# Performance work log

Measured on AMD Instinct MI355X. Metric: run time of the kernel, lower is better.

## Reference

```python
import jax, jax.numpy as jnp
from jax import lax
import numpy as np

EPS = 2.220446049250313e-16  # sys.float_info.epsilon


def setup_inputs() -> dict:
    key = jax.random.key(0)
    k1, k2, k3, k4 = jax.random.split(key, 4)
    C, H, W, R = 256, 256, 256, 16
    x = jax.random.normal(k1, (1, C, H, W), dtype=jnp.float32)
    w1 = jax.random.normal(k2, (R, C), dtype=jnp.float32) * 0.05   # Linear(C -> C//r), no bias
    w2 = jax.random.normal(k3, (C, R), dtype=jnp.float32) * 0.05   # Linear(C//r -> C), no bias
    conv_w = jax.random.normal(k4, (1, 2, 7, 7), dtype=jnp.float32) * 0.05  # Conv2d(2,1,7)
    return {"x": x, "w1": w1, "w2": w2, "conv_w": conv_w, "kv": 1}


def reference(x, w1, w2, conv_w, kv):
    b, c, h, w = x.shape  # b == 1 (module assumes batch 1 via squeeze(0))

    def fc(v):  # shared MLP of the channel attention
        return jnp.maximum(v @ w1.T, 0.0) @ w2.T

    y_avg = fc(x.mean(axis=(2, 3)))          # [1, C]
    y_max = fc(x.max(axis=(2, 3)))           # [1, C]
    y = jax.nn.sigmoid(y_avg + y_max)        # [1, C]

    yc = y[0]
    yc = (yc - yc.min()) / (yc.max() - yc.min() + 1e-20)  # min-max normalized gates in [0,1]

    # Batched SVD over channels replaces the per-channel Python loop.
    mats = x[0]                                            # [C, H, W]
    u, s, vh = jnp.linalg.svd(mats, full_matrices=False)   # u:[C,H,K] s:[C,K] vh:[C,K,W]
    K = s.shape[-1]
    # k = int(len(s) * kv * yc[c]); singular values are sorted descending, so
    # top-k selection == keep the first k -> mask the tail.
    k = jnp.floor(K * kv * yc).astype(jnp.int32)           # [C]
    keep = jnp.arange(K)[None, :] < k[:, None]             # [C, K]
    s_m = jnp.where(keep, s, 0.0)
    recon = jnp.einsum('chk,ck,ckw->chw', u, s_m, vh)      # low-rank reconstruction
    x2 = recon[None]                                       # [1, C, H, W]

    avg_out = x2.mean(axis=1, keepdims=True)
    max_out = x2.max(axis=1, keepdims=True)
    cat = jnp.concatenate([avg_out, max_out], axis=1)      # [1, 2, H, W]
    out = lax.conv_general_dilated(cat, conv_w, (1, 1), [(3, 3), (3, 3)],
                                   dimension_numbers=('NCHW', 'OIHW', 'NCHW'))
    out = jnp.where(out < EPS, EPS, out)
    return jax.nn.sigmoid(out)
```

## Files before the change

### kernel.cpp

```cpp
#include <hip/hip_runtime.h>


#define NCH 256
#define N 256
#define NN 65536
#define NS_MAX 22

#define OFF_K 0
#define OFF_MODE 256
#define OFF_MC 512
#define OFF_COEF 768
#define OFF_SUM 12032
#define OFF_MAXHW 77568
#define OFF_MEAND 143104
#define OFF_MAXD 143616
#define OFF_T 144128
#define OFF_ALPHA 144640
#define OFF_AQ 145152
#define OFF_BQ 276224
#define OFF_ITSW 407296
#define SMALL_FLOATS 407552

#define NSH_LDS 135168
#define F16_PANEL 33792

#define P_TOTAL 33280

static const float EPSF = 2.220446049250313e-16f;

typedef unsigned short u16;
typedef _Float16 h8 __attribute__((ext_vector_type(8)));
typedef float f32x4 __attribute__((ext_vector_type(4)));

__device__ __forceinline__ float rdlane(float v, int l) {
  return __uint_as_float(__builtin_amdgcn_readlane(__float_as_uint(v), l));
}

__device__ __forceinline__ int offP(int rr) {
  int q = rr >> 2, s = rr & 3;
  return 4 * (q + 1) * (2 * q + s);
}

__device__ __forceinline__ u16 f2h(float v) {
  _Float16 h = (_Float16)v;
  u16 u;
  __builtin_memcpy(&u, &h, 2);
  return u;
}
__device__ __forceinline__ float h2f(u16 u) {
  _Float16 h;
  __builtin_memcpy(&h, &u, 2);
  return (float)h;
}

__device__ __forceinline__ double block_sum1024d(double v, double* red, int tid) {
  for (int off = 32; off; off >>= 1) v += __shfl_down(v, off, 64);
  __syncthreads();
  if ((tid & 63) == 0) red[tid >> 6] = v;
  __syncthreads();
  double s = 0.0;
#pragma unroll
  for (int i = 0; i < 16; ++i) s += red[i];
  return s;
}

__global__ __launch_bounds__(256) void k_chan_stats(const float* __restrict__ x,
                                                    float* __restrict__ small) {
  int c = blockIdx.x, tid = threadIdx.x;
  const float4* xc = (const float4*)(x + (size_t)c * NN);
  double s = 0.0;
  float m = -1e30f;
  for (int i = tid; i < NN / 4; i += 256) {
    float4 v = xc[i];
    s += (double)v.x + (double)v.y + (double)v.z + (double)v.w;
    m = fmaxf(m, fmaxf(fmaxf(v.x, v.y), fmaxf(v.z, v.w)));
  }
  __shared__ double rs[4];
  __shared__ float rm[4];
  for (int off = 32; off; off >>= 1) {
    s += __shfl_down(s, off, 64);
    m = fmaxf(m, __shfl_down(m, off, 64));
  }
  if ((tid & 63) == 0) { rs[tid >> 6] = s; rm[tid >> 6] = m; }
  __syncthreads();
  if (tid == 0) {
    ((double*)(small + OFF_MEAND))[c] = (rs[0] + rs[1] + rs[2] + rs[3]) / (double)NN;
    ((double*)(small + OFF_MAXD))[c] =
        (double)fmaxf(fmaxf(rm[0], rm[1]), fmaxf(rm[2], rm[3]));
  }
}

__global__ __launch_bounds__(256) void k_attention(const float* __restrict__ w1,
                                                   const float* __restrict__ w2,
                                                   const int* __restrict__ kvp,
                                                   float* __restrict__ small) {
  int tid = threadIdx.x;
  __shared__ double ha[16], hm[16], redd[8], ymn[256], ymx[256];
  double va = ((const double*)(small + OFF_MEAND))[tid];
  double vm = ((const double*)(small + OFF_MAXD))[tid];
  for (int r = 0; r < 16; ++r) {
    double wv = (double)w1[r * 256 + tid];
    double pa = wv * va, pm = wv * vm;
    for (int off = 32; off; off >>= 1) {
      pa += __shfl_down(pa, off, 64);
      pm += __shfl_down(pm, off, 64);
    }
    if ((tid & 63) == 0) { redd[tid >> 6] = pa; redd[4 + (tid >> 6)] = pm; }
    __syncthreads();
    if (tid == 0) {
      ha[r] = fmax(redd[0] + redd[1] + redd[2] + redd[3], 0.0);
      hm[r] = fmax(redd[4] + redd[5] + redd[6] + redd[7], 0.0);
    }
    __syncthreads();
  }
  double ya = 0.0, ym = 0.0;
  for (int r = 0; r < 16; ++r) {
    double wv = (double)w2[tid * 16 + r];
    ya += ha[r] * wv;
    ym += hm[r] * wv;
  }
  double y = 1.0 / (1.0 + exp(-(ya + ym)));
  ymn[tid] = y; ymx[tid] = y;
  __syncthreads();
  for (int off = 128; off; off >>= 1) {
    if (tid < off) {
      ymn[tid] = fmin(ymn[tid], ymn[tid + off]);
      ymx[tid] = fmax(ymx[tid], ymx[tid + off]);
    }
    __syncthreads();
  }
  double yc = (y - ymn[0]) / (ymx[0] - ymn[0] + 1e-20);
  int kv = kvp[0];
  int k = (int)floor(256.0 * (double)kv * yc);
  int mode = (k <= 0) ? 0 : ((k >= 256) ? 1 : 2);
  int* ip = (int*)small;
  ip[OFF_K + tid] = k;
  ip[OFF_MODE + tid] = mode;
}

#define GEMM128_VARS                                                           \
  int tid = threadIdx.x;                                                       \
  int tx4 = (tid & 15) * 4, ty4 = (tid >> 4) * 4;                              \
  int lm = tid >> 1, lq = (tid & 1) * 2;                                       \
  int lk = tid >> 4, lc = (tid & 15) * 2;                                      \
  (void)lk; (void)lc;

#define STORE_T128(Ls, v0, v1)                                                 \
  Ls[lq * 4 + 0][lm] = v0.x; Ls[lq * 4 + 1][lm] = v0.y;                        \
  Ls[lq * 4 + 2][lm] = v0.z; Ls[lq * 4 + 3][lm] = v0.w;                        \
  Ls[lq * 4 + 4][lm] = v1.x; Ls[lq * 4 + 5][lm] = v1.y;                        \
  Ls[lq * 4 + 6][lm] = v1.z; Ls[lq * 4 + 7][lm] = v1.w;

#define GEMM128_INNER(AsM, BsM)                                                \
  _Pragma("unroll") for (int kk = 0; kk < 16; ++kk) {                          \
    float4 a0 = *(const float4*)&AsM[kk][ty4];                                 \
    float4 a1 = *(const float4*)&AsM[kk][64 + ty4];                            \
    float4 b0 = *(const float4*)&BsM[kk][tx4];                                 \
    float4 b1 = *(const float4*)&BsM[kk][64 + tx4];                            \
    float av[8] = {a0.x, a0.y, a0.z, a0.w, a1.x, a1.y, a1.z, a1.w};            \
    float bv[8] = {b0.x, b0.y, b0.z, b0.w, b1.x, b1.y, b1.z, b1.w};            \
    _Pragma("unroll") for (int rr = 0; rr < 8; ++rr)                           \
      _Pragma("unroll") for (int cc2 = 0; cc2 < 8; ++cc2)                      \
        acc[rr][cc2] += av[rr] * bv[cc2];                                      \
  }

#define WRITE_TILE_NORM(Cc)                                                    \
  _Pragma("unroll") for (int rh = 0; rh < 2; ++rh)                             \
  _Pragma("unroll") for (int rr = 0; rr < 4; ++rr) {                           \
    int rI = rh * 4 + rr;                                                      \
    float* rowp = (Cc) + (size_t)(i0 + rh * 64 + ty4 + rr) * N + j0;           \
    *(float4*)(rowp + tx4) =                                                   \
        make_float4(acc[rI][0], acc[rI][1], acc[rI][2], acc[rI][3]);           \
    *(float4*)(rowp + 64 + tx4) =                                              \
        make_float4(acc[rI][4], acc[rI][5], acc[rI][6], acc[rI][7]);           \
  }

#define WRITE_TILE_MIRROR(Cc)                                                  \
  _Pragma("unroll") for (int ch = 0; ch < 2; ++ch)                             \
  _Pragma("unroll") for (int cc2 = 0; cc2 < 4; ++cc2) {                        \
    int cI = ch * 4 + cc2;                                                     \
    float* rowp = (Cc) + (size_t)(j0 + ch * 64 + tx4 + cc2) * N + i0;          \
    *(float4*)(rowp + ty4) =                                                   \
        make_float4(acc[0][cI], acc[1][cI], acc[2][cI], acc[3][cI]);           \
    *(float4*)(rowp + 64 + ty4) =                                              \
        make_float4(acc[4][cI], acc[5][cI], acc[6][cI], acc[7][cI]);           \
  }

#define SYM_MAP                                                                \
  int bx = blockIdx.x;                                                         \
  int i0 = (bx >= 1) ? 128 : 0, j0 = (bx == 2) ? 128 : 0;

__global__ __launch_bounds__(256) void k_gram(const float* __restrict__ x,
                                              float* __restrict__ bufA, int base) {
  __shared__ float As[16][132], Bs[16][132];
  GEMM128_VARS; SYM_MAP;
  const float* A = x + (size_t)(base + blockIdx.z) * NN;
  float acc[8][8] = {};
  const float* Ap = A + (size_t)(i0 + lm) * N + lq * 4;
  const float* Bp = A + (size_t)(j0 + lm) * N + lq * 4;
  float4 va0 = *(const float4*)Ap, va1 = *(const float4*)(Ap + 4);
  float4 vb0 = *(const float4*)Bp, vb1 = *(const float4*)(Bp + 4);
  for (int kt = 0; kt < 16; ++kt) {
    __syncthreads();
    STORE_T128(As, va0, va1); STORE_T128(Bs, vb0, vb1);
    __syncthreads();
    if (kt < 15) {
      va0 = *(const float4*)(Ap + (kt + 1) * 16);
      va1 = *(const float4*)(Ap + (kt + 1) * 16 + 4);
      vb0 = *(const float4*)(Bp + (kt + 1) * 16);
      vb1 = *(const float4*)(Bp + (kt + 1) * 16 + 4);
    }
    GEMM128_INNER(As, Bs);
  }
  float* Cc = bufA + (size_t)blockIdx.z * NN;
  WRITE_TILE_NORM(Cc);
  if (bx == 1) { WRITE_TILE_MIRROR(Cc); }
}

__global__ __launch_bounds__(1024) void k_tridiag(const float* __restrict__ Gall,
                                                  float* __restrict__ small, int base) {
  extern __shared__ double dls[];
  double* redd = dls;
  double* wd = dls + 16;
  double* pip = dls + 272;
  float* P = (float*)(dls + 1296);
  float* uf = P + P_TOTAL;
  int tid = threadIdx.x, lane = tid & 63;
  int r = tid & 255, g = tid >> 8;
  int R0 = ((tid >> 6) & 3) << 6;
  int c = base + blockIdx.x;
  const int* ip = (const int*)small;
  if (ip[OFF_MODE + c] != 2) return;
  const float* G = Gall + (size_t)blockIdx.x * NN;
  double* aq = (double*)(small + OFF_AQ) + (size_t)c * 256;
  double* bq = (double*)(small + OFF_BQ) + (size_t)c * 256;
  const int offR = offP(r);

  for (int i = g; i < N; i += 4)
    if (r <= i) P[offP(i) + r] = G[i * N + r];
  __syncthreads();

  for (int j = 0; j + 2 < N; ++j) {
    if (g == 0 && r >= j + 1) uf[r] = P[offR + j];
    __syncthreads();
    float ur0 = uf[r];
    double part = (g == 0 && r >= j + 2) ? (double)ur0 * (double)ur0 : 0.0;
    double x0 = (double)uf[j + 1];
    double sigma = block_sum1024d(part, redd, tid);
    if (sigma <= 1e-40) {
      if (tid == 0) bq[j] = x0;
      __syncthreads();
      continue;
    }
    double nu = sqrt(x0 * x0 + sigma);
    double bsub = (x0 >= 0.0) ? -nu : nu;
    double beta = 1.0 / (nu * (nu + fabs(x0)));
    if (tid == j + 1) uf[tid] = (float)(x0 - bsub);
    __syncthreads();
    int cbase = (j + 1) & ~63;
    int c0 = cbase + 64 * g;
    float ureg = 0.f;
    if (c0 < N) ureg = uf[c0 + lane];
    double myp = 0.0;
    if (c0 < N) {
      int lbeg = (c0 > j + 1) ? c0 : (j + 1);
      int lend = c0 + 64;
      if (lbeg < lend) {
        double pi0 = 0.0, pi1 = 0.0, pi2 = 0.0, pi3 = 0.0;
        if (c0 + 64 <= R0) {
          int lmv = lbeg;
          for (; lmv < lend && (lmv & 3); ++lmv) {
            float uv = rdlane(ureg, lmv - c0);
            pi0 += (double)P[offR + lmv] * (double)uv;
          }
          for (; lmv + 3 < lend; lmv += 4) {
            float4 v4 = *(const float4*)&P[offR + lmv];
            float uv0 = rdlane(ureg, lmv - c0), uv1 = rdlane(ureg, lmv + 1 - c0);
            float uv2 = rdlane(ureg, lmv + 2 - c0), uv3 = rdlane(ureg, lmv + 3 - c0);
            pi0 += (double)v4.x * (double)uv0;
            pi1 += (double)v4.y * (double)uv1;
            pi2 += (double)v4.z * (double)uv2;
            pi3 += (double)v4.w * (double)uv3;
          }
        } else if (c0 >= R0 + 64) {
          int lmv = lbeg;
          int oL = offP(lbeg);
          for (; lmv + 3 < lend; lmv += 4) {
            int o0 = oL;
            int o1 = o0 + ((lmv + 4) & ~3);
            int o2 = o1 + ((lmv + 5) & ~3);
            int o3 = o2 + ((lmv + 6) & ~3);
            oL = o3 + ((lmv + 7) & ~3);
            float uv0 = rdlane(ureg, lmv - c0), uv1 = rdlane(ureg, lmv + 1 - c0);
            float uv2 = rdlane(ureg, lmv + 2 - c0), uv3 = rdlane(ureg, lmv + 3 - c0);
            pi0 += (double)P[o0 + r] * (double)uv0;
            pi1 += (double)P[o1 + r] * (double)uv1;
            pi2 += (double)P[o2 + r] * (double)uv2;
            pi3 += (double)P[o3 + r] * (double)uv3;
          }
          for (; lmv < lend; ++lmv) {
            float uv = rdlane(ureg, lmv - c0);
            pi0 += (double)P[oL + r] * (double)uv;
            oL += (lmv + 4) & ~3;
          }
        } else {
          for (int lmv = lbeg; lmv < lend; ++lmv) {
            float uv = rdlane(ureg, lmv - c0);
            float v = P[(lmv <= r) ? (offR + lmv) : (offP(lmv) + r)];
            pi0 += (double)v * (double)uv;
          }
        }
        myp = (pi0 + pi1) + (pi2 + pi3);
      }
    }
    pip[tid] = (r >= j + 1) ? myp : 0.0;
    __syncthreads();
    double ur = (r >= j + 1) ? (double)uf[r] : 0.0;
    double pi = 0.0;
    if (g == 0 && r >= j + 1)
      pi = (pip[r] + pip[256 + r] + pip[512 + r] + pip[768 + r]) * beta;
    double kpart = (g == 0) ? ur * pi : 0.0;
    double K = block_sum1024d(kpart, redd, tid) * beta * 0.5;
    if (g == 0) wd[r] = pi - K * ur;
    __syncthreads();
    if (c0 < N && r >= j + 1) {
      double wr = wd[r];
      int lbeg = (c0 > j + 1) ? c0 : (j + 1);
      int lend = c0 + 64;
      int lcap = (r | 63) + 1;
      if (lend > lcap) lend = lcap;
      if (c0 + 64 <= R0) {
        int lmv = lbeg;
        for (; lmv < lend && (lmv & 3); ++lmv) {
          double uv = (double)rdlane(ureg, lmv - c0), wv = wd[lmv];
          P[offR + lmv] = (float)((double)P[offR + lmv] - ur * wv - wr * uv);
        }
        for (; lmv + 3 < lend; lmv += 4) {
          float4 p4 = *(float4*)&P[offR + lmv];
          double uv0 = (double)rdlane(ureg, lmv - c0), wv0 = wd[lmv];
          double uv1 = (double)rdlane(ureg, lmv + 1 - c0), wv1 = wd[lmv + 1];
          double uv2 = (double)rdlane(ureg, lmv + 2 - c0), wv2 = wd[lmv + 2];
          double uv3 = (double)rdlane(ureg, lmv + 3 - c0), wv3 = wd[lmv + 3];
          p4.x = (float)((double)p4.x - ur * wv0 - wr * uv0);
          p4.y = (float)((double)p4.y - ur * wv1 - wr * uv1);
          p4.z = (float)((double)p4.z - ur * wv2 - wr * uv2);
          p4.w = (float)((double)p4.w - ur * wv3 - wr * uv3);
          *(float4*)&P[offR + lmv] = p4;
        }
      } else if (c0 == R0) {
        for (int lmv = lbeg; lmv < lend; ++lmv) {
          double uv = (double)rdlane(ureg, lmv - c0), wv = wd[lmv];
          if (lmv <= r)
            P[offR + lmv] = (float)((double)P[offR + lmv] - ur * wv - wr * uv);
        }
      }
    }
    if (tid == 0) bq[j] = bsub;
    __syncthreads();
  }
  if (g == 0) aq[r] = (double)P[offR + r];
  if (tid == 0) bq[N - 2] = (double)P[offP(N - 1) + N - 2];
}

__device__ __forceinline__ int sturm_count_lds(const double* a, const double* b,
                                               double t) {
  double d = a[0] - t;
  int cnt = (d < 0.0);
  for (int i = 1; i < N; ++i) {
    double den = d;
    if (fabs(den) < 1e-20) den = (den < 0.0) ? -1e-20 : 1e-20;
    double bb = b[i - 1];
    d = (a[i] - t) - bb * bb / den;
    cnt += (d < 0.0);
  }
  return cnt;
}

__global__ __launch_bounds__(64) void k_bisect(float* __restrict__ small,
                                               int base, int cc) {
  int ci = blockIdx.x;
  if (ci >= cc) return;
  int c = base + ci, lane = threadIdx.x;
  int* ip = (int*)small;
  if (ip[OFF_MODE + c] != 2) {
    if (lane == 0) { ip[OFF_MC + c] = 0; ip[OFF_ITSW + c] = 0; }
    return;
  }
  int k = ip[OFF_K + c];
  const double* a = (const double*)(small + OFF_AQ) + (size_t)c * 256;
  const double* b = (const double*)(small + OFF_BQ) + (size_t)c * 256;
  __shared__ double sa[256], sb[256];
  for (int i = lane; i < N; i += 64) {
    sa[i] = a[i];
    if (i < N - 1) sb[i] = b[i];
  }
  __syncthreads();
  double lo = 1e300, hi = -1e300;
  for (int i = lane; i < N; i += 64) {
    double rr = (i > 0 ? fabs(sb[i - 1]) : 0.0) + (i < N - 1 ? fabs(sb[i]) : 0.0);
    lo = fmin(lo, sa[i] - rr);
    hi = fmax(hi, sa[i] + rr);
  }
  for (int off = 32; off; off >>= 1) {
    lo = fmin(lo, __shfl_xor(lo, off, 64));
    hi = fmax(hi, __shfl_xor(hi, off, 64));
  }
  double lamk = 0.0, lamk1 = 0.0;
  for (int which = 0; which < 2; ++which) {
    int j = (which == 0) ? (N - k + 1) : (N - k);
    double l0 = lo, h0 = hi;
    for (int pass = 0; pass < 10; ++pass) {
      double step = (h0 - l0) * (1.0 / 65.0);
      double t = l0 + step * (double)(lane + 1);
      int cnt = sturm_count_lds(sa, sb, t);
      unsigned long long mask = __ballot(cnt >= j);
      if (mask == 0ull) {
        l0 = l0 + step * 64.0;
      } else {
        int bpos = __ffsll((long long)mask) - 1;
        double nl = (bpos == 0) ? l0 : (l0 + step * (double)bpos);
        h0 = l0 + step * (double)(bpos + 1);
        l0 = nl;
      }
    }
    double v = 0.5 * (l0 + h0);
    if (which == 0) lamk = v; else lamk1 = v;
  }
  if (lane == 0) {
    double t = 0.5 * (lamk + lamk1);
    double gap = fmax(lamk - lamk1, 0.0);
    double alpha = 1.002 * fmax(hi - t, t - lo) + 1e-30;
    double g0 = fmax(gap / (2.0 * alpha), 2e-6);
    float* cf = small + OFF_COEF + (size_t)c * (2 * NS_MAX);
    double l = fmin(g0, 0.99);
    int m = 0, isw = NS_MAX;
    while (m < NS_MAX - 2 && l < 0.9999) {
      if (isw == NS_MAX && l >= 0.04) isw = m;
      double aa = sqrt(27.0 / (4.0 * (1.0 + l + l * l)));
      double bb = (4.0 / 27.0) * aa * aa * aa;
      cf[2 * m] = (float)aa;
      cf[2 * m + 1] = (float)bb;
      double pl = aa * l - bb * l * l * l;
      double p1 = aa - bb;
      l = fmin(pl, p1);
      m++;
    }
    for (int e = 0; e < 2; ++e) {
      if (isw == NS_MAX && l >= 0.04) isw = m;
      cf[2 * m] = 1.5f; cf[2 * m + 1] = 0.5f; m++;
    }
    if (isw > m) isw = m;
    ip[OFF_MC + c] = m;
    ip[OFF_ITSW + c] = isw;
    ((double*)(small + OFF_T))[c] = t;
    ((double*)(small + OFF_ALPHA))[c] = alpha;
  }
}

__global__ void k_x0(const float* __restrict__ small, float* __restrict__ bufA,
                     int base) {
  int ci = blockIdx.y, c = base + ci;
  const int* ip = (const int*)small;
  if (ip[OFF_MODE + c] != 2) return;
  double t = ((const double*)(small + OFF_T))[c];
  double inva = 1.0 / ((const double*)(small + OFF_ALPHA))[c];
  float* X = bufA + (size_t)ci * NN;
  int r = blockIdx.x, tid = threadIdx.x;
  double gg = (double)X[r * N + tid];
  if (tid == r) gg -= t;
  X[r * N + tid] = (float)(gg * inva);
}

__global__ __launch_bounds__(256) void k_ns1(const float* __restrict__ src,
                                             float* __restrict__ Sb,
                                             const float* __restrict__ small,
                                             int base, int it) {
  const int* ip = (const int*)small;
  int c = base + blockIdx.z;
  if (ip[OFF_MODE + c] != 2 || it >= ip[OFF_ITSW + c]) return;
  __shared__ float As[16][132], Bs[16][132];
  GEMM128_VARS; SYM_MAP;
  const float* X = src + (size_t)blockIdx.z * NN;
  float acc[8][8] = {};
  const float* Ap = X + (size_t)(i0 + lm) * N + lq * 4;
  const float* Bp = X + (size_t)(j0 + lm) * N + lq * 4;
  float4 va0 = *(const float4*)Ap, va1 = *(const float4*)(Ap + 4);
  float4 vb0 = *(const float4*)Bp, vb1 = *(const float4*)(Bp + 4);
  for (int kt = 0; kt < 16; ++kt) {
    __syncthreads();
    STORE_T128(As, va0, va1); STORE_T128(Bs, vb0, vb1);
    __syncthreads();
    if (kt < 15) {
      va0 = *(const float4*)(Ap + (kt + 1) * 16);
      va1 = *(const float4*)(Ap + (kt + 1) * 16 + 4);
      vb0 = *(const float4*)(Bp + (kt + 1) * 16);
      vb1 = *(const float4*)(Bp + (kt + 1) * 16 + 4);
    }
    GEMM128_INNER(As, Bs);
  }
  float* Cc = Sb + (size_t)blockIdx.z * NN;
  WRITE_TILE_NORM(Cc);
  if (bx == 1) { WRITE_TILE_MIRROR(Cc); }
}

__global__ __launch_bounds__(256) void k_ns2(const float* __restrict__ src,
                                             const float* __restrict__ Sb,
                                             float* __restrict__ dst,
                                             const float* __restrict__ small,
                                             int base, int it) {
  const int* ip = (const int*)small;
  int c = base + blockIdx.z;
  if (ip[OFF_MODE + c] != 2 || it >= ip[OFF_ITSW + c]) return;
  float ca = small[OFF_COEF + (size_t)c * (2 * NS_MAX) + 2 * it];
  float cb = small[OFF_COEF + (size_t)c * (2 * NS_MAX) + 2 * it + 1];
  __shared__ float As[16][132], Bs[16][132];
  GEMM128_VARS; SYM_MAP;
  const float* X = src + (size_t)blockIdx.z * NN;
  const float* S = Sb + (size_t)blockIdx.z * NN;
  float acc[8][8] = {};
  const float* Ap = X + (size_t)(i0 + lm) * N + lq * 4;
  const float* Bp = S + (size_t)(j0 + lm) * N + lq * 4;
  float4 va0 = *(const float4*)Ap, va1 = *(const float4*)(Ap + 4);
  float4 vb0 = *(const float4*)Bp, vb1 = *(const float4*)(Bp + 4);
  for (int kt = 0; kt < 16; ++kt) {
    __syncthreads();
    STORE_T128(As, va0, va1); STORE_T128(Bs, vb0, vb1);
    __syncthreads();
    if (kt < 15) {
      va0 = *(const float4*)(Ap + (kt + 1) * 16);
      va1 = *(const float4*)(Ap + (kt + 1) * 16 + 4);
      vb0 = *(const float4*)(Bp + (kt + 1) * 16);
      vb1 = *(const float4*)(Bp + (kt + 1) * 16 + 4);
    }
    GEMM128_INNER(As, Bs);
  }
#pragma unroll
  for (int rh = 0; rh < 2; ++rh)
#pragma unroll
    for (int rr = 0; rr < 4; ++rr) {
      int rI = rh * 4 + rr;
      const float* rowp = X + (size_t)(i0 + rh * 64 + ty4 + rr) * N + j0;
      float4 x0 = *(const float4*)(rowp + tx4);
      float4 x1 = *(const float4*)(rowp + 64 + tx4);
      acc[rI][0] = ca * x0.x - cb * acc[rI][0];
      acc[rI][1] = ca * x0.y - cb * acc[rI][1];
      acc[rI][2] = ca * x0.z - cb * acc[rI][2];
      acc[rI][3] = ca * x0.w - cb * acc[rI][3];
      acc[rI][4] = ca * x1.x - cb * acc[rI][4];
      acc[rI][5] = ca * x1.y - cb * acc[rI][5];
      acc[rI][6] = ca * x1.z - cb * acc[rI][6];
      acc[rI][7] = ca * x1.w - cb * acc[rI][7];
    }
  float* Y = dst + (size_t)blockIdx.z * NN;
  WRITE_TILE_NORM(Y);
  if (bx == 1) { WRITE_TILE_MIRROR(Y); }
}

__device__ __forceinline__ void stage_h(u16* pan, const u16* g16, int tid) {
#pragma unroll
  for (int i = 0; i < 16; ++i) {
    int g = tid * 16 + i * 4096;
    int lo = g + ((g >> 9) << 4);
    *(uint4*)((char*)pan + lo) = *(const uint4*)((const char*)g16 + g);
  }
}
__device__ __forceinline__ void stage_f(u16* pan, const float* gF, int tid) {
#pragma unroll
  for (int i = 0; i < 16; ++i) {
    int e = tid * 8 + i * 2048;
    float4 v0 = *(const float4*)(gF + e);
    float4 v1 = *(const float4*)(gF + e + 4);
    h8 hv;
    hv[0] = (_Float16)v0.x; hv[1] = (_Float16)v0.y;
    hv[2] = (_Float16)v0.z; hv[3] = (_Float16)v0.w;
    hv[4] = (_Float16)v1.x; hv[5] = (_Float16)v1.y;
    hv[6] = (_Float16)v1.z; hv[7] = (_Float16)v1.w;
    int b = e * 2;
    int lo = b + ((b >> 9) << 4);
    *(h8*)((char*)pan + lo) = hv;
  }
}

__global__ __launch_bounds__(256) void k_nsh(const float* __restrict__ srcF,
                                             float* __restrict__ Sf,
                                             float* __restrict__ dstF,
                                             const float* __restrict__ small,
                                             int base, int it, int phase) {
  const int* ip = (const int*)small;
  int ci = blockIdx.z, c = base + ci;
  if (ip[OFF_MODE + c] != 2) return;
  int isw = ip[OFF_ITSW + c], mc = ip[OFF_MC + c];
  if (it < isw || it >= mc) return;
  SYM_MAP;
  extern __shared__ char ldsraw[];
  u16* Apan = (u16*)ldsraw;
  u16* Bpan = Apan + F16_PANEL;
  int tid = threadIdx.x;
  bool cvtA = (it == isw);
  bool sameP = (phase == 0) && (bx != 1);
  const float* XF = srcF + (size_t)ci * NN;
  const u16* XH = (const u16*)XF;
  if (cvtA) stage_f(Apan, XF + (size_t)i0 * N, tid);
  else      stage_h(Apan, XH + (size_t)i0 * N, tid);
  if (!sameP) {
    if (phase == 0) {
      if (cvtA) stage_f(Bpan, XF + (size_t)j0 * N, tid);
      else      stage_h(Bpan, XH + (size_t)j0 * N, tid);
    } else {
      const u16* SH = (const u16*)(Sf + (size_t)ci * NN);
      stage_h(Bpan, SH + (size_t)j0 * N, tid);
    }
  }
  const u16* Bb = sameP ? Apan : Bpan;
  __syncthreads();

  int l = tid & 63, wid = tid >> 6;
  int wr = (wid >> 1) * 64, wc = (wid & 1) * 64;
  int rA = wr + (l & 15), rB = wc + (l & 15);
  int kB = (l >> 4) << 3;
  f32x4 zero = {0.f, 0.f, 0.f, 0.f};
  f32x4 acc[4][4];
#pragma unroll
  for (int mi = 0; mi < 4; ++mi)
#pragma unroll
    for (int ni = 0; ni < 4; ++ni) acc[mi][ni] = zero;

#pragma unroll
  for (int kc = 0; kc < 8; ++kc) {
    int kof = kc * 32 + kB;
    h8 af[4], bf[4];
#pragma unroll
    for (int mi = 0; mi < 4; ++mi)
      af[mi] = *(const h8*)((const char*)Apan +
                            ((size_t)(rA + mi * 16) * 264 + kof) * 2);
#pragma unroll
    for (int ni = 0; ni < 4; ++ni)
      bf[ni] = *(const h8*)((const char*)Bb +
                            ((size_t)(rB + ni * 16) * 264 + kof) * 2);
#pragma unroll
    for (int mi = 0; mi < 4; ++mi)
#pragma unroll
      for (int ni = 0; ni < 4; ++ni)
        acc[mi][ni] = __builtin_amdgcn_mfma_f32_16x16x32_f16(
            af[mi], bf[ni], acc[mi][ni], 0, 0, 0);
  }

  float cav = 0.f, cbv = 0.f;
  bool last = false;
  if (phase) {
    cav = small[OFF_COEF + (size_t)c * (2 * NS_MAX) + 2 * it];
    cbv = small[OFF_COEF + (size_t)c * (2 * NS_MAX) + 2 * it + 1];
    last = (it == mc - 1);
  }
  float* oF = dstF + (size_t)ci * NN;
  u16* oH = phase ? (u16*)oF : (u16*)(Sf + (size_t)ci * NN);
  int lr4 = (l >> 4) << 2, lcn = l & 15;
#pragma unroll
  for (int mi = 0; mi < 4; ++mi)
#pragma unroll
    for (int ni = 0; ni < 4; ++ni)
#pragma unroll
      for (int rg = 0; rg < 4; ++rg) {
        int gr = i0 + wr + mi * 16 + lr4 + rg;
        int gc = j0 + wc + ni * 16 + lcn;
        float v = acc[mi][ni][rg];
        if (phase) {
          float xv = h2f(Apan[(size_t)(gr - i0) * 264 + gc]);
          v = cav * xv - cbv * v;
        }
        if (!last) {
          u16 hv = f2h(v);
          oH[(size_t)gr * N + gc] = hv;
          if (bx == 1) oH[(size_t)gc * N + gr] = hv;
        } else {
          oF[(size_t)gr * N + gc] = v;
          if (bx == 1) oF[(size_t)gc * N + gr] = v;
        }
      }
}

__global__ __launch_bounds__(256) void k_proj(const float* __restrict__ bufA,
                                              const float* __restrict__ bufB,
                                              const float* __restrict__ x,
                                              float* __restrict__ bufC,
                                              const float* __restrict__ small,
                                              int base) {
  const int* ip = (const int*)small;
  int ci = blockIdx.z, c = base + ci;
  int mode = ip[OFF_MODE + c];
  GEMM128_VARS;
  int i0 = blockIdx.x * 128, j0 = blockIdx.y * 128;
  float* Cc = bufC + (size_t)ci * NN;
  const float* xc = x + (size_t)c * NN;
  if (mode != 2) {
#pragma unroll
    for (int rh = 0; rh < 2; ++rh)
#pragma unroll
      for (int rr = 0; rr < 4; ++rr) {
        size_t ro = (size_t)(i0 + rh * 64 + ty4 + rr) * N + j0;
        if (mode == 0) {
          *(float4*)(Cc + ro + tx4) = make_float4(0.f, 0.f, 0.f, 0.f);
          *(float4*)(Cc + ro + 64 + tx4) = make_float4(0.f, 0.f, 0.f, 0.f);
        } else {
          *(float4*)(Cc + ro + tx4) = *(const float4*)(xc + ro + tx4);
          *(float4*)(Cc + ro + 64 + tx4) = *(const float4*)(xc + ro + 64 + tx4);
        }
      }
    return;
  }
  int mc = ip[OFF_MC + c];
  const float* Xh = ((mc & 1) ? bufB : bufA) + (size_t)ci * NN;
  __shared__ float As[16][132], Bs[16][132];
  float acc[8][8] = {};
  const float* Ap = Xh + (size_t)(i0 + lm) * N + lq * 4;
  const float* Bp = xc + (size_t)lk * N + j0 + lc * 4;
  float4 va0 = *(const float4*)Ap, va1 = *(const float4*)(Ap + 4);
  float4 vb0 = *(const float4*)Bp, vb1 = *(const float4*)(Bp + 4);
  for (int kt = 0; kt < 16; ++kt) {
    __syncthreads();
    STORE_T128(As, va0, va1);
    *(float4*)&Bs[lk][lc * 4] = vb0;
    *(float4*)&Bs[lk][(lc + 1) * 4] = vb1;
    __syncthreads();
    if (kt < 15) {
      va0 = *(const float4*)(Ap + (kt + 1) * 16);
      va1 = *(const float4*)(Ap + (kt + 1) * 16 + 4);
      const float* Bp2 = xc + (size_t)((kt + 1) * 16 + lk) * N + j0 + lc * 4;
      vb0 = *(const float4*)Bp2;
      vb1 = *(const float4*)(Bp2 + 4);
    }
    GEMM128_INNER(As, Bs);
  }
#pragma unroll
  for (int rh = 0; rh < 2; ++rh)
#pragma unroll
    for (int rr = 0; rr < 4; ++rr) {
      int rI = rh * 4 + rr;
      const float* rowp = xc + (size_t)(i0 + rh * 64 + ty4 + rr) * N + j0;
      float4 x0 = *(const float4*)(rowp + tx4);
      float4 x1 = *(const float4*)(rowp + 64 + tx4);
      acc[rI][0] = 0.5f * (acc[rI][0] + x0.x);
      acc[rI][1] = 0.5f * (acc[rI][1] + x0.y);
      acc[rI][2] = 0.5f * (acc[rI][2] + x0.z);
      acc[rI][3] = 0.5f * (acc[rI][3] + x0.w);
      acc[rI][4] = 0.5f * (acc[rI][4] + x1.x);
      acc[rI][5] = 0.5f * (acc[rI][5] + x1.y);
      acc[rI][6] = 0.5f * (acc[rI][6] + x1.z);
      acc[rI][7] = 0.5f * (acc[rI][7] + x1.w);
    }
  WRITE_TILE_NORM(Cc);
}

__global__ void k_accum(const float* __restrict__ bufC, float* __restrict__ sum_hw,
                        float* __restrict__ max_hw, int cc, int first) {
  int p = blockIdx.x * 256 + threadIdx.x;
  float s = first ? 0.f : sum_hw[p];
  float m = first ? -1e30f : max_hw[p];
  for (int ci = 0; ci < cc; ++ci) {
    float v = bufC[(size_t)ci * NN + p];
    s += v;
    m = fmaxf(m, v);
  }
  sum_hw[p] = s;
  max_hw[p] = m;
}

__global__ void k_conv(const float* __restrict__ sum_hw, const float* __restrict__ max_hw,
                       const float* __restrict__ cw, float* __restrict__ out) {
  int p = blockIdx.x * 256 + threadIdx.x;
  int h = p >> 8, w = p & 255;
  float acc = 0.f;
  for (int dy = 0; dy < 7; ++dy) {
    int hy = h + dy - 3;
    if (hy < 0 || hy > 255) continue;
    for (int dx = 0; dx < 7; ++dx) {
      int wx = w + dx - 3;
      if (wx < 0 || wx > 255) continue;
      int q = hy * 256 + wx;
      acc += cw[dy * 7 + dx] * (sum_hw[q] * (1.f / 256.f)) +
             cw[49 + dy * 7 + dx] * max_hw[q];
    }
  }
  acc = fmaxf(acc, EPSF);
  out[p] = 1.f / (1.f + expf(-acc));
}

extern "C" void kernel_launch(void* const* d_in, const int* in_sizes, int n_in,
                              void* d_out, int out_size, void* d_ws, size_t ws_size,
                              hipStream_t stream) {
  const float* x = (const float*)d_in[0];
  const float* w1 = (const float*)d_in[1];
  const float* w2 = (const float*)d_in[2];
  const float* cw = (const float*)d_in[3];
  const int* kv = (const int*)d_in[4];
  float* out = (float*)d_out;
  float* small = (float*)d_ws;

  size_t small_bytes = (size_t)SMALL_FLOATS * 4;
  size_t avail = ws_size > small_bytes ? ws_size - small_bytes : 0;
  long chunk = (long)(avail / (3ull * NN * 4));
  if (chunk > NCH) chunk = NCH;
  if (chunk < 1) chunk = 1;
  float* bufA = small + SMALL_FLOATS;
  float* bufB = bufA + (size_t)chunk * NN;
  float* bufC = bufB + (size_t)chunk * NN;

  const int tridiag_lds = 1296 * 8 + P_TOTAL * 4 + 256 * 4;
  hipFuncSetAttribute((const void*)k_tridiag,
                      hipFuncAttributeMaxDynamicSharedMemorySize, tridiag_lds);
  hipFuncSetAttribute((const void*)k_nsh,
                      hipFuncAttributeMaxDynamicSharedMemorySize, NSH_LDS);

  k_chan_stats<<<NCH, 256, 0, stream>>>(x, small);
  k_attention<<<1, 256, 0, stream>>>(w1, w2, kv, small);

  const int IT32 = 13;

  for (int base = 0; base < NCH; base += (int)chunk) {
    int cc = (NCH - base < (int)chunk) ? (NCH - base) : (int)chunk;
    dim3 gsym(3, 1, cc);
    dim3 gproj(2, 2, cc);
    k_gram<<<gsym, 256, 0, stream>>>(x, bufA, base);
    k_tridiag<<<cc, 1024, tridiag_lds, stream>>>(bufA, small, base);
    k_bisect<<<cc, 64, 0, stream>>>(small, base, cc);
    k_x0<<<dim3(N, cc), 256, 0, stream>>>(small, bufA, base);
    for (int it = 0; it < NS_MAX; ++it) {
      const float* src = (it & 1) ? bufB : bufA;
      float* dst = (it & 1) ? bufA : bufB;
      if (it < IT32) {
        k_ns1<<<gsym, 256, 0, stream>>>(src, bufC, small, base, it);
        k_ns2<<<gsym, 256, 0, stream>>>(src, bufC, dst, small, base, it);
      }
      k_nsh<<<gsym, 256, NSH_LDS, stream>>>(src, bufC, dst, small, base, it, 0);
      k_nsh<<<gsym, 256, NSH_LDS, stream>>>(src, bufC, dst, small, base, it, 1);
    }
    k_proj<<<gproj, 256, 0, stream>>>(bufA, bufB, x, bufC, small, base);
    k_accum<<<256, 256, 0, stream>>>(bufC, small + OFF_SUM, small + OFF_MAXHW, cc,
                                     base == 0 ? 1 : 0);
  }
  k_conv<<<256, 256, 0, stream>>>(small + OFF_SUM, small + OFF_MAXHW, cw, out);
}
```

Baseline: 6.797 ms.

## Repad packed triangle layout in tridiag LDS and broadcast row offsets/w via readlane

Changes the packed lower-triangular LDS storage of the Householder tridiagonalization to a new padded row-offset scheme held in a lookup table, with row strides padded (likely to cut LDS bank conflicts). Row offsets and the w vector are now loaded once per wave and broadcast with readlane rather than recomputed or re-read from LDS in the inner loops. This adds about 14 KB of LDS per block and extra scalar readlane traffic, including two readlanes per double.

```diff
diff --git a/kernel.cpp b/kernel.cpp
--- a/kernel.cpp
+++ b/kernel.cpp
@@ -24,7 +24,7 @@
 #define NSH_LDS 135168
 #define F16_PANEL 33792
 
-#define P_TOTAL 33280
+#define P_TOTAL 36864
 
 static const float EPSF = 2.220446049250313e-16f;
 
@@ -35,10 +35,16 @@
 __device__ __forceinline__ float rdlane(float v, int l) {
   return __uint_as_float(__builtin_amdgcn_readlane(__float_as_uint(v), l));
 }
-
-__device__ __forceinline__ int offP(int rr) {
-  int q = rr >> 2, s = rr & 3;
-  return 4 * (q + 1) * (2 * q + s);
+__device__ __forceinline__ int rdlane_i(int v, int l) {
+  return __builtin_amdgcn_readlane(v, l);
+}
+__device__ __forceinline__ double rdlane_d(double v, int l) {
+  union { double d; unsigned long long u; } x;
+  x.d = v;
+  unsigned lo = __builtin_amdgcn_readlane((unsigned)x.u, l);
+  unsigned hi = __builtin_amdgcn_readlane((unsigned)(x.u >> 32), l);
+  x.u = ((unsigned long long)hi << 32) | lo;
+  return x.d;
 }
 
 __device__ __forceinline__ u16 f2h(float v) {
@@ -225,6 +231,7 @@
   double* pip = dls + 272;
   float* P = (float*)(dls + 1296);
   float* uf = P + P_TOTAL;
+  int* roL = (int*)(uf + 256);
   int tid = threadIdx.x, lane = tid & 63;
   int r = tid & 255, g = tid >> 8;
   int R0 = ((tid >> 6) & 3) << 6;
@@ -234,10 +241,21 @@
   const float* G = Gall + (size_t)blockIdx.x * NN;
   double* aq = (double*)(small + OFF_AQ) + (size_t)c * 256;
   double* bq = (double*)(small + OFF_BQ) + (size_t)c * 256;
-  const int offR = offP(r);
+
+  if (tid < 256) {
+    int rr = tid, v;
+    if (rr < 4) v = rr * 4;
+    else {
+      int m = rr - 4, gq = m >> 5, s = m & 31;
+      v = 16 + 1152 * gq + 512 * gq * (gq - 1) + s * (36 + 32 * gq);
+    }
+    roL[rr] = v;
+  }
+  __syncthreads();
+  const int offR = roL[r];
 
   for (int i = g; i < N; i += 4)
-    if (r <= i) P[offP(i) + r] = G[i * N + r];
+    if (r <= i) P[roL[i] + r] = G[i * N + r];
   __syncthreads();
 
   for (int j = 0; j + 2 < N; ++j) {
@@ -260,7 +278,8 @@
     int cbase = (j + 1) & ~63;
     int c0 = cbase + 64 * g;
     float ureg = 0.f;
-    if (c0 < N) ureg = uf[c0 + lane];
+    int roreg = 0;
+    if (c0 < N) { ureg = uf[c0 + lane]; roreg = roL[c0 + lane]; }
     double myp = 0.0;
     if (c0 < N) {
       int lbeg = (c0 > j + 1) ? c0 : (j + 1);
@@ -284,29 +303,27 @@
           }
         } else if (c0 >= R0 + 64) {
           int lmv = lbeg;
-          int oL = offP(lbeg);
           for (; lmv + 3 < lend; lmv += 4) {
-            int o0 = oL;
-            int o1 = o0 + ((lmv + 4) & ~3);
-            int o2 = o1 + ((lmv + 5) & ~3);
-            int o3 = o2 + ((lmv + 6) & ~3);
-            oL = o3 + ((lmv + 7) & ~3);
+            int o0 = rdlane_i(roreg, lmv - c0) + r;
+            int o1 = rdlane_i(roreg, lmv + 1 - c0) + r;
+            int o2 = rdlane_i(roreg, lmv + 2 - c0) + r;
+            int o3 = rdlane_i(roreg, lmv + 3 - c0) + r;
             float uv0 = rdlane(ureg, lmv - c0), uv1 = rdlane(ureg, lmv + 1 - c0);
             float uv2 = rdlane(ureg, lmv + 2 - c0), uv3 = rdlane(ureg, lmv + 3 - c0);
-            pi0 += (double)P[o0 + r] * (double)uv0;
-            pi1 += (double)P[o1 + r] * (double)uv1;
-            pi2 += (double)P[o2 + r] * (double)uv2;
-            pi3 += (double)P[o3 + r] * (double)uv3;
+            pi0 += (double)P[o0] * (double)uv0;
+            pi1 += (double)P[o1] * (double)uv1;
+            pi2 += (double)P[o2] * (double)uv2;
+            pi3 += (double)P[o3] * (double)uv3;
           }
           for (; lmv < lend; ++lmv) {
             float uv = rdlane(ureg, lmv - c0);
-            pi0 += (double)P[oL + r] * (double)uv;
-            oL += (lmv + 4) & ~3;
+            pi0 += (double)P[rdlane_i(roreg, lmv - c0) + r] * (double)uv;
           }
         } else {
           for (int lmv = lbeg; lmv < lend; ++lmv) {
             float uv = rdlane(ureg, lmv - c0);
-            float v = P[(lmv <= r) ? (offR + lmv) : (offP(lmv) + r)];
+            int oc = rdlane_i(roreg, lmv - c0) + r;
+            float v = P[(lmv <= r) ? (offR + lmv) : oc];
             pi0 += (double)v * (double)uv;
           }
         }
@@ -323,6 +340,8 @@
     double K = block_sum1024d(kpart, redd, tid) * beta * 0.5;
     if (g == 0) wd[r] = pi - K * ur;
     __syncthreads();
+    double wreg = 0.0;
+    if (c0 < N) wreg = wd[c0 + lane];
     if (c0 < N && r >= j + 1) {
       double wr = wd[r];
       int lbeg = (c0 > j + 1) ? c0 : (j + 1);
@@ -332,15 +351,16 @@
       if (c0 + 64 <= R0) {
         int lmv = lbeg;
         for (; lmv < lend && (lmv & 3); ++lmv) {
-          double uv = (double)rdlane(ureg, lmv - c0), wv = wd[lmv];
+          double uv = (double)rdlane(ureg, lmv - c0);
+          double wv = rdlane_d(wreg, lmv - c0);
           P[offR + lmv] = (float)((double)P[offR + lmv] - ur * wv - wr * uv);
         }
         for (; lmv + 3 < lend; lmv += 4) {
           float4 p4 = *(float4*)&P[offR + lmv];
-          double uv0 = (double)rdlane(ureg, lmv - c0), wv0 = wd[lmv];
-          double uv1 = (double)rdlane(ureg, lmv + 1 - c0), wv1 = wd[lmv + 1];
-          double uv2 = (double)rdlane(ureg, lmv + 2 - c0), wv2 = wd[lmv + 2];
-          double uv3 = (double)rdlane(ureg, lmv + 3 - c0), wv3 = wd[lmv + 3];
+          double uv0 = (double)rdlane(ureg, lmv - c0), wv0 = rdlane_d(wreg, lmv - c0);
+          double uv1 = (double)rdlane(ureg, lmv + 1 - c0), wv1 = rdlane_d(wreg, lmv + 1 - c0);
+          double uv2 = (double)rdlane(ureg, lmv + 2 - c0), wv2 = rdlane_d(wreg, lmv + 2 - c0);
+          double uv3 = (double)rdlane(ureg, lmv + 3 - c0), wv3 = rdlane_d(wreg, lmv + 3 - c0);
           p4.x = (float)((double)p4.x - ur * wv0 - wr * uv0);
           p4.y = (float)((double)p4.y - ur * wv1 - wr * uv1);
           p4.z = (float)((double)p4.z - ur * wv2 - wr * uv2);
@@ -349,7 +369,8 @@
         }
       } else if (c0 == R0) {
         for (int lmv = lbeg; lmv < lend; ++lmv) {
-          double uv = (double)rdlane(ureg, lmv - c0), wv = wd[lmv];
+          double uv = (double)rdlane(ureg, lmv - c0);
+          double wv = rdlane_d(wreg, lmv - c0);
           if (lmv <= r)
             P[offR + lmv] = (float)((double)P[offR + lmv] - ur * wv - wr * uv);
         }
@@ -359,7 +380,7 @@
     __syncthreads();
   }
   if (g == 0) aq[r] = (double)P[offR + r];
-  if (tid == 0) bq[N - 2] = (double)P[offP(N - 1) + N - 2];
+  if (tid == 0) bq[N - 2] = (double)P[roL[N - 1] + N - 2];
 }
 
 __device__ __forceinline__ int sturm_count_lds(const double* a, const double* b,
@@ -805,7 +826,7 @@
   float* bufB = bufA + (size_t)chunk * NN;
   float* bufC = bufB + (size_t)chunk * NN;
 
-  const int tridiag_lds = 1296 * 8 + P_TOTAL * 4 + 256 * 4;
+  const int tridiag_lds = 1296 * 8 + P_TOTAL * 4 + 256 * 4 + 256 * 4;
   hipFuncSetAttribute((const void*)k_tridiag,
                       hipFuncAttributeMaxDynamicSharedMemorySize, tridiag_lds);
   hipFuncSetAttribute((const void*)k_nsh,
```

After: 6.367 ms. 1.07x faster.

## Pack tridiagonalization in plain triangle, fp32 rank-2 update, earlier precision switch

Applied to the files above, without the earlier changes.

The Householder tridiagonalization kernel now stores the symmetric matrix as a plain packed lower triangle instead of the padded 4-aligned layout. This drops float4 vector loads but shrinks LDS. The rank-2 update now runs in fp32 FMAs, with the w vector broadcast through readlane instead of read as doubles from LDS, which cuts double-precision ALU work. Separately, the Newton-Schulz switch threshold drops from 0.04 to 0.02, so the iteration moves to its later phase sooner. That may save iterations but risks accuracy, as does the fp32 update.

```diff
diff --git a/kernel.cpp b/kernel.cpp
--- a/kernel.cpp
+++ b/kernel.cpp
@@ -24,8 +24,6 @@
 #define NSH_LDS 135168
 #define F16_PANEL 33792
 
-#define P_TOTAL 33280
-
 static const float EPSF = 2.220446049250313e-16f;
 
 typedef unsigned short u16;
@@ -34,11 +32,6 @@
 
 __device__ __forceinline__ float rdlane(float v, int l) {
   return __uint_as_float(__builtin_amdgcn_readlane(__float_as_uint(v), l));
-}
-
-__device__ __forceinline__ int offP(int rr) {
-  int q = rr >> 2, s = rr & 3;
-  return 4 * (q + 1) * (2 * q + s);
 }
 
 __device__ __forceinline__ u16 f2h(float v) {
@@ -221,10 +214,10 @@
                                                   float* __restrict__ small, int base) {
   extern __shared__ double dls[];
   double* redd = dls;
-  double* wd = dls + 16;
-  double* pip = dls + 272;
-  float* P = (float*)(dls + 1296);
-  float* uf = P + P_TOTAL;
+  double* pip = dls + 16;
+  float* P = (float*)(dls + 1040);
+  float* uf = P + 32896;
+  float* wf = uf + 256;
   int tid = threadIdx.x, lane = tid & 63;
   int r = tid & 255, g = tid >> 8;
   int R0 = ((tid >> 6) & 3) << 6;
@@ -234,14 +227,14 @@
   const float* G = Gall + (size_t)blockIdx.x * NN;
   double* aq = (double*)(small + OFF_AQ) + (size_t)c * 256;
   double* bq = (double*)(small + OFF_BQ) + (size_t)c * 256;
-  const int offR = offP(r);
+  const int triR = (r * (r + 1)) >> 1;
 
   for (int i = g; i < N; i += 4)
-    if (r <= i) P[offP(i) + r] = G[i * N + r];
+    if (r <= i) P[((i * (i + 1)) >> 1) + r] = G[i * N + r];
   __syncthreads();
 
   for (int j = 0; j + 2 < N; ++j) {
-    if (g == 0 && r >= j + 1) uf[r] = P[offR + j];
+    if (g == 0 && r >= j + 1) uf[r] = P[triR + j];
     __syncthreads();
     float ur0 = uf[r];
     double part = (g == 0 && r >= j + 2) ? (double)ur0 * (double)ur0 : 0.0;
@@ -269,45 +262,43 @@
         double pi0 = 0.0, pi1 = 0.0, pi2 = 0.0, pi3 = 0.0;
         if (c0 + 64 <= R0) {
           int lmv = lbeg;
-          for (; lmv < lend && (lmv & 3); ++lmv) {
-            float uv = rdlane(ureg, lmv - c0);
-            pi0 += (double)P[offR + lmv] * (double)uv;
-          }
           for (; lmv + 3 < lend; lmv += 4) {
-            float4 v4 = *(const float4*)&P[offR + lmv];
             float uv0 = rdlane(ureg, lmv - c0), uv1 = rdlane(ureg, lmv + 1 - c0);
             float uv2 = rdlane(ureg, lmv + 2 - c0), uv3 = rdlane(ureg, lmv + 3 - c0);
-            pi0 += (double)v4.x * (double)uv0;
-            pi1 += (double)v4.y * (double)uv1;
-            pi2 += (double)v4.z * (double)uv2;
-            pi3 += (double)v4.w * (double)uv3;
+            float v0 = P[triR + lmv], v1 = P[triR + lmv + 1];
+            float v2 = P[triR + lmv + 2], v3 = P[triR + lmv + 3];
+            pi0 += (double)v0 * (double)uv0;
+            pi1 += (double)v1 * (double)uv1;
+            pi2 += (double)v2 * (double)uv2;
+            pi3 += (double)v3 * (double)uv3;
           }
+          for (; lmv < lend; ++lmv)
+            pi0 += (double)P[triR + lmv] * (double)rdlane(ureg, lmv - c0);
         } else if (c0 >= R0 + 64) {
           int lmv = lbeg;
-          int oL = offP(lbeg);
+          int s = (lmv * (lmv + 1)) >> 1;
           for (; lmv + 3 < lend; lmv += 4) {
-            int o0 = oL;
-            int o1 = o0 + ((lmv + 4) & ~3);
-            int o2 = o1 + ((lmv + 5) & ~3);
-            int o3 = o2 + ((lmv + 6) & ~3);
-            oL = o3 + ((lmv + 7) & ~3);
+            int s0 = s, s1 = s0 + lmv + 1, s2 = s1 + lmv + 2, s3 = s2 + lmv + 3;
+            s = s3 + lmv + 4;
             float uv0 = rdlane(ureg, lmv - c0), uv1 = rdlane(ureg, lmv + 1 - c0);
             float uv2 = rdlane(ureg, lmv + 2 - c0), uv3 = rdlane(ureg, lmv + 3 - c0);
-            pi0 += (double)P[o0 + r] * (double)uv0;
-            pi1 += (double)P[o1 + r] * (double)uv1;
-            pi2 += (double)P[o2 + r] * (double)uv2;
-            pi3 += (double)P[o3 + r] * (double)uv3;
+            pi0 += (double)P[s0 + r] * (double)uv0;
+            pi1 += (double)P[s1 + r] * (double)uv1;
+            pi2 += (double)P[s2 + r] * (double)uv2;
+            pi3 += (double)P[s3 + r] * (double)uv3;
           }
           for (; lmv < lend; ++lmv) {
-            float uv = rdlane(ureg, lmv - c0);
-            pi0 += (double)P[oL + r] * (double)uv;
-            oL += (lmv + 4) & ~3;
+            pi0 += (double)P[s + r] * (double)rdlane(ureg, lmv - c0);
+            s += lmv + 1;
           }
         } else {
-          for (int lmv = lbeg; lmv < lend; ++lmv) {
+          int lmv = lbeg;
+          int s = (lmv * (lmv + 1)) >> 1;
+          for (; lmv < lend; ++lmv) {
             float uv = rdlane(ureg, lmv - c0);
-            float v = P[(lmv <= r) ? (offR + lmv) : (offP(lmv) + r)];
+            float v = P[(lmv <= r) ? (triR + lmv) : (s + r)];
             pi0 += (double)v * (double)uv;
+            s += lmv + 1;
           }
         }
         myp = (pi0 + pi1) + (pi2 + pi3);
@@ -321,45 +312,42 @@
       pi = (pip[r] + pip[256 + r] + pip[512 + r] + pip[768 + r]) * beta;
     double kpart = (g == 0) ? ur * pi : 0.0;
     double K = block_sum1024d(kpart, redd, tid) * beta * 0.5;
-    if (g == 0) wd[r] = pi - K * ur;
-    __syncthreads();
+    if (g == 0) wf[r] = (float)(pi - K * ur);
+    __syncthreads();
+    float wreg = 0.f;
+    if (c0 < N) wreg = wf[c0 + lane];
     if (c0 < N && r >= j + 1) {
-      double wr = wd[r];
+      float urf = uf[r];
+      float wrf = wf[r];
       int lbeg = (c0 > j + 1) ? c0 : (j + 1);
       int lend = c0 + 64;
       int lcap = (r | 63) + 1;
       if (lend > lcap) lend = lcap;
       if (c0 + 64 <= R0) {
         int lmv = lbeg;
-        for (; lmv < lend && (lmv & 3); ++lmv) {
-          double uv = (double)rdlane(ureg, lmv - c0), wv = wd[lmv];
-          P[offR + lmv] = (float)((double)P[offR + lmv] - ur * wv - wr * uv);
+        for (; lmv + 1 < lend; lmv += 2) {
+          float uv0 = rdlane(ureg, lmv - c0), wv0 = rdlane(wreg, lmv - c0);
+          float uv1 = rdlane(ureg, lmv + 1 - c0), wv1 = rdlane(wreg, lmv + 1 - c0);
+          P[triR + lmv] = fmaf(-wrf, uv0, fmaf(-urf, wv0, P[triR + lmv]));
+          P[triR + lmv + 1] = fmaf(-wrf, uv1, fmaf(-urf, wv1, P[triR + lmv + 1]));
         }
-        for (; lmv + 3 < lend; lmv += 4) {
-          float4 p4 = *(float4*)&P[offR + lmv];
-          double uv0 = (double)rdlane(ureg, lmv - c0), wv0 = wd[lmv];
-          double uv1 = (double)rdlane(ureg, lmv + 1 - c0), wv1 = wd[lmv + 1];
-          double uv2 = (double)rdlane(ureg, lmv + 2 - c0), wv2 = wd[lmv + 2];
-          double uv3 = (double)rdlane(ureg, lmv + 3 - c0), wv3 = wd[lmv + 3];
-          p4.x = (float)((double)p4.x - ur * wv0 - wr * uv0);
-          p4.y = (float)((double)p4.y - ur * wv1 - wr * uv1);
-          p4.z = (float)((double)p4.z - ur * wv2 - wr * uv2);
-          p4.w = (float)((double)p4.w - ur * wv3 - wr * uv3);
-          *(float4*)&P[offR + lmv] = p4;
+        if (lmv < lend) {
+          float uv0 = rdlane(ureg, lmv - c0), wv0 = rdlane(wreg, lmv - c0);
+          P[triR + lmv] = fmaf(-wrf, uv0, fmaf(-urf, wv0, P[triR + lmv]));
         }
       } else if (c0 == R0) {
         for (int lmv = lbeg; lmv < lend; ++lmv) {
-          double uv = (double)rdlane(ureg, lmv - c0), wv = wd[lmv];
+          float uv = rdlane(ureg, lmv - c0), wv = rdlane(wreg, lmv - c0);
           if (lmv <= r)
-            P[offR + lmv] = (float)((double)P[offR + lmv] - ur * wv - wr * uv);
+            P[triR + lmv] = fmaf(-wrf, uv, fmaf(-urf, wv, P[triR + lmv]));
         }
       }
     }
     if (tid == 0) bq[j] = bsub;
     __syncthreads();
   }
-  if (g == 0) aq[r] = (double)P[offR + r];
-  if (tid == 0) bq[N - 2] = (double)P[offP(N - 1) + N - 2];
+  if (g == 0) aq[r] = (double)P[triR + r];
+  if (tid == 0) bq[N - 2] = (double)P[(((N - 1) * N) >> 1) + N - 2];
 }
 
 __device__ __forceinline__ int sturm_count_lds(const double* a, const double* b,
@@ -435,7 +423,7 @@
     double l = fmin(g0, 0.99);
     int m = 0, isw = NS_MAX;
     while (m < NS_MAX - 2 && l < 0.9999) {
-      if (isw == NS_MAX && l >= 0.04) isw = m;
+      if (isw == NS_MAX && l >= 0.02) isw = m;
       double aa = sqrt(27.0 / (4.0 * (1.0 + l + l * l)));
       double bb = (4.0 / 27.0) * aa * aa * aa;
       cf[2 * m] = (float)aa;
@@ -446,7 +434,7 @@
       m++;
     }
     for (int e = 0; e < 2; ++e) {
-      if (isw == NS_MAX && l >= 0.04) isw = m;
+      if (isw == NS_MAX && l >= 0.02) isw = m;
       cf[2 * m] = 1.5f; cf[2 * m + 1] = 0.5f; m++;
     }
     if (isw > m) isw = m;
@@ -805,7 +793,7 @@
   float* bufB = bufA + (size_t)chunk * NN;
   float* bufC = bufB + (size_t)chunk * NN;
 
-  const int tridiag_lds = 1296 * 8 + P_TOTAL * 4 + 256 * 4;
+  const int tridiag_lds = 1040 * 8 + 32896 * 4 + 512 * 4;
   hipFuncSetAttribute((const void*)k_tridiag,
                       hipFuncAttributeMaxDynamicSharedMemorySize, tridiag_lds);
   hipFuncSetAttribute((const void*)k_nsh,
```

Result: faster. 5.786 ms (-14.9%).
